# Performance work log

Measured on AMD Instinct MI355X. Metric: run time of the kernel, lower is better.

The kernel has to match this reference:

```python
import jax, jax.numpy as jnp
import numpy as np

NEG_INF = -1.0e9  # matches the torch code's -1000000000.0 fill


def setup_inputs() -> dict:
    key = jax.random.key(0)
    k1, k2, k3, k4 = jax.random.split(key, 4)
    B, Lq, Lk, D = 8, 2048, 2048, 128
    queries = jax.random.normal(k1, (B, Lq, D), dtype=jnp.float32)
    keys = jax.random.normal(k2, (B, Lk, D), dtype=jnp.float32)
    values = jax.random.normal(k3, (B, Lk, D), dtype=jnp.float32)
    valid_length = jax.random.randint(k4, (B,), 1, Lk + 1, dtype=jnp.int32)
    return {"queries": queries, "keys": keys, "values": values,
            "valid_length": valid_length}


def reference(queries, keys, values, valid_length):
    d = queries.shape[-1]
    # scores: [B, Lq, Lk]
    scores = jnp.einsum("bqd,bkd->bqk", queries, keys) / jnp.sqrt(
        jnp.asarray(d, dtype=queries.dtype))
    # per-batch valid key length broadcast over all queries
    Lk = scores.shape[-1]
    mask = jnp.arange(Lk)[None, None, :] >= valid_length[:, None, None]  # [B,1,Lk]
    scores = jnp.where(mask, NEG_INF, scores)
    attn = jax.nn.softmax(scores, axis=-1)
    # dropout p=0.0 -> identity (eval-equivalent)
    return jnp.einsum("bqk,bkd->bqd", attn, values)
```

## Files before the change

### kernel.cpp

```cpp
#include <hip/hip_runtime.h>


#define NB     8
#define LQ     2048
#define LK     2048
#define DH     128
#define KT     32
#define NSPLIT 4
#define CHUNK  512
#define TPS    16
#define NTILES 64
#define SCL2E  0.12751744f

typedef float f32x4 __attribute__((ext_vector_type(4)));
typedef __bf16 bf16x8 __attribute__((ext_vector_type(8)));
typedef unsigned short u16x4 __attribute__((ext_vector_type(4)));
typedef unsigned short u16x8 __attribute__((ext_vector_type(8)));
typedef unsigned int u32x4 __attribute__((ext_vector_type(4)));

#define KWS_OFF   0ull
#define VWS_OFF   (4ull << 20)
#define OPART_OFF (8ull << 20)
#define ML_OFF    (OPART_OFF + (32ull << 20))
#define WS_NEED   (ML_OFF + 262144ull)

static __device__ __forceinline__ unsigned short f2bf(float f) {
    unsigned int u = __builtin_bit_cast(unsigned int, f);
    u += 0x7FFFu + ((u >> 16) & 1u);
    return (unsigned short)(u >> 16);
}

static __device__ __forceinline__ unsigned int cvtpk(float lo, float hi) {
    unsigned int r;
    asm("v_cvt_pk_bf16_f32 %0, %1, %2" : "=v"(r) : "v"(lo), "v"(hi));
    return r;
}

__global__ __launch_bounds__(256)
void prepass(const float* __restrict__ Kg, const float* __restrict__ Vg,
             const int* __restrict__ VLg,
             unsigned short* __restrict__ Kws, unsigned short* __restrict__ Vws) {
    __shared__ unsigned short Kl[KT][136];
    __shared__ unsigned short Vt[DH][40];
    const int tid = threadIdx.x;
    const int b = blockIdx.x >> 6;
    const int t = blockIdx.x & 63;
    if (t * KT >= VLg[b]) return;
    const size_t gbase = ((size_t)b * LK + (size_t)t * KT) * DH;
    const size_t tbase = (size_t)(b * NTILES + t) * 4096;
    #pragma unroll
    for (int i = 0; i < 4; ++i) {
        int e4 = tid + 256 * i;
        int row = e4 >> 5;
        int c4 = (e4 & 31) * 4;
        float4 kv = *reinterpret_cast<const float4*>(Kg + gbase + (size_t)row * DH + c4);
        u16x4 uk = { f2bf(kv.x), f2bf(kv.y), f2bf(kv.z), f2bf(kv.w) };
        *reinterpret_cast<u16x4*>(&Kl[row][c4]) = uk;
        float4 vv = *reinterpret_cast<const float4*>(Vg + gbase + (size_t)row * DH + c4);
        Vt[c4 + 0][row] = f2bf(vv.x);
        Vt[c4 + 1][row] = f2bf(vv.y);
        Vt[c4 + 2][row] = f2bf(vv.z);
        Vt[c4 + 3][row] = f2bf(vv.w);
    }
    __syncthreads();
    #pragma unroll
    for (int i = 0; i < 2; ++i) {
        int u = tid + 256 * i;
        int sl = u >> 6;
        int l = u & 63;
        int krow = 2 * (l & 15) + (sl & 1);
        int kcol = (sl >> 1) * 32 + (l >> 4) * 8;
        u16x8 kk = *reinterpret_cast<const u16x8*>(&Kl[krow][kcol]);
        *reinterpret_cast<u16x8*>(Kws + tbase + u * 8) = kk;
        int vcol = sl * 16 + (l & 15);
        int k0 = (l >> 4) * 8;
        u16x8 vv8 = *reinterpret_cast<const u16x8*>(&Vt[vcol][k0]);
        *reinterpret_cast<u16x8*>(Vws + tbase + u * 8) = vv8;
    }
}

__global__ __launch_bounds__(128, 2)
void attn_split(const float* __restrict__ Qg, const int* __restrict__ VLg,
                const unsigned short* __restrict__ Kws,
                const unsigned short* __restrict__ Vws,
                float* __restrict__ Opart, float* __restrict__ Ml,
                float* __restrict__ Og) {
    __shared__ __align__(16) char shbuf[16640];

    const int tid  = threadIdx.x;
    const int lane = tid & 63;
    const int wv   = tid >> 6;
    const int r    = lane & 15;
    const int grp  = lane >> 4;

    unsigned short* Plds = reinterpret_cast<unsigned short*>(shbuf) + wv * 1280;

    const int bid = blockIdx.x;
    const int b  = bid >> 8;
    const int s  = (bid >> 6) & 3;
    const int qb = bid & 63;

    const int vl = VLg[b];
    if (s * CHUNK >= vl) return;
    int vrem = vl - s * CHUNK;
    if (vrem > CHUNK) vrem = CHUNK;
    const int nt = (vrem + 31) >> 5;
    const bool anymask = (vrem & 31) != 0;
    const int q0 = qb * 32;

    bf16x8 qf0[4], qf1[4];
    #pragma unroll
    for (int rb = 0; rb < 2; ++rb) {
        const float* qrow = Qg + ((size_t)(b * LQ + q0 + rb * 16 + r)) * DH + grp * 8;
        #pragma unroll
        for (int c = 0; c < 4; ++c) {
            float4 f0 = *reinterpret_cast<const float4*>(qrow + c * 32);
            float4 f1 = *reinterpret_cast<const float4*>(qrow + c * 32 + 4);
            u32x4 tw;
            tw[0] = cvtpk(f0.x * SCL2E, f0.y * SCL2E);
            tw[1] = cvtpk(f0.z * SCL2E, f0.w * SCL2E);
            tw[2] = cvtpk(f1.x * SCL2E, f1.y * SCL2E);
            tw[3] = cvtpk(f1.z * SCL2E, f1.w * SCL2E);
            if (rb == 0) qf0[c] = __builtin_bit_cast(bf16x8, tw);
            else         qf1[c] = __builtin_bit_cast(bf16x8, tw);
        }
    }

    const f32x4 zero4 = {0.f, 0.f, 0.f, 0.f};
    f32x4 acc[2][8];
    #pragma unroll
    for (int rb = 0; rb < 2; ++rb)
        #pragma unroll
        for (int d8 = 0; d8 < 8; ++d8) acc[rb][d8] = zero4;
    float lsum[2][4] = {{0.f, 0.f, 0.f, 0.f}, {0.f, 0.f, 0.f, 0.f}};

    const unsigned short* kp =
        Kws + (size_t)(b * NTILES + s * TPS + wv) * 4096 + lane * 8;
    const unsigned short* vp =
        Vws + (size_t)(b * NTILES + s * TPS + wv) * 4096 + lane * 8;

    bf16x8 kreg[8], vreg[8];
    #pragma unroll
    for (int sl = 0; sl < 8; ++sl) {
        kreg[sl] = *reinterpret_cast<const bf16x8*>(kp + sl * 512);
        vreg[sl] = *reinterpret_cast<const bf16x8*>(vp + sl * 512);
    }

    for (int t = wv; t < nt; t += 2) {
        const bool lastt = (t == nt - 1);
        f32x4 s00 = zero4, s01 = zero4, s10 = zero4, s11 = zero4;
        #pragma unroll
        for (int c = 0; c < 4; ++c) {
            s00 = __builtin_amdgcn_mfma_f32_16x16x32_bf16(qf0[c], kreg[2 * c],     s00, 0, 0, 0);
            s01 = __builtin_amdgcn_mfma_f32_16x16x32_bf16(qf0[c], kreg[2 * c + 1], s01, 0, 0, 0);
            s10 = __builtin_amdgcn_mfma_f32_16x16x32_bf16(qf1[c], kreg[2 * c],     s10, 0, 0, 0);
            s11 = __builtin_amdgcn_mfma_f32_16x16x32_bf16(qf1[c], kreg[2 * c + 1], s11, 0, 0, 0);
        }
        if (t + 2 < nt) {
            kp += 2 * 4096;
            #pragma unroll
            for (int sl = 0; sl < 8; ++sl)
                kreg[sl] = *reinterpret_cast<const bf16x8*>(kp + sl * 512);
        }

        const int kk = s * CHUNK + t * KT + 2 * r;
        const bool mm = lastt & anymask;
        const bool m0 = mm && (kk >= vl);
        const bool m1 = mm && (kk + 1 >= vl);
        #pragma unroll
        for (int j = 0; j < 4; ++j) {
            float a0 = m0 ? -1e9f : s00[j];
            float a1 = m1 ? -1e9f : s01[j];
            float b0 = m0 ? -1e9f : s10[j];
            float b1 = m1 ? -1e9f : s11[j];
            float p00 = exp2f(a0), p01 = exp2f(a1);
            float p10 = exp2f(b0), p11 = exp2f(b1);
            lsum[0][j] += p00 + p01;
            lsum[1][j] += p10 + p11;
            *reinterpret_cast<unsigned int*>(&Plds[(grp * 4 + j) * 40 + 2 * r]) =
                cvtpk(p00, p01);
            *reinterpret_cast<unsigned int*>(&Plds[640 + (grp * 4 + j) * 40 + 2 * r]) =
                cvtpk(p10, p11);
        }
        bf16x8 pa0 = *reinterpret_cast<const bf16x8*>(&Plds[r * 40 + grp * 8]);
        bf16x8 pa1 = *reinterpret_cast<const bf16x8*>(&Plds[640 + r * 40 + grp * 8]);

        #pragma unroll
        for (int d8 = 0; d8 < 8; ++d8) {
            acc[0][d8] = __builtin_amdgcn_mfma_f32_16x16x32_bf16(pa0, vreg[d8], acc[0][d8], 0, 0, 0);
            acc[1][d8] = __builtin_amdgcn_mfma_f32_16x16x32_bf16(pa1, vreg[d8], acc[1][d8], 0, 0, 0);
        }
        if (t + 2 < nt) {
            vp += 2 * 4096;
            #pragma unroll
            for (int sl = 0; sl < 8; ++sl)
                vreg[sl] = *reinterpret_cast<const bf16x8*>(vp + sl * 512);
        }
    }

    #pragma unroll
    for (int rb = 0; rb < 2; ++rb) {
        #pragma unroll
        for (int j = 0; j < 4; ++j) {
            float v = lsum[rb][j];
            #pragma unroll
            for (int d = 1; d < 16; d <<= 1) v += __shfl_xor(v, d);
            lsum[rb][j] = v;
        }
    }

    __syncthreads();
    float* Cmb = reinterpret_cast<float*>(shbuf);
    float* Ls  = reinterpret_cast<float*>(shbuf + 16384);
    if (wv == 1) {
        #pragma unroll
        for (int rb = 0; rb < 2; ++rb) {
            #pragma unroll
            for (int d8 = 0; d8 < 8; ++d8) {
                int ps = ((rb * 8 + d8) + lane) & 15;
                *reinterpret_cast<f32x4*>(&Cmb[lane * 64 + ps * 4]) = acc[rb][d8];
            }
        }
        if (r == 0) {
            #pragma unroll
            for (int rb = 0; rb < 2; ++rb)
                #pragma unroll
                for (int j = 0; j < 4; ++j)
                    Ls[rb * 16 + grp * 4 + j] = lsum[rb][j];
        }
    }
    __syncthreads();
    if (wv != 0) return;

    #pragma unroll
    for (int rb = 0; rb < 2; ++rb) {
        #pragma unroll
        for (int d8 = 0; d8 < 8; ++d8) {
            int ps = ((rb * 8 + d8) + lane) & 15;
            f32x4 o = *reinterpret_cast<const f32x4*>(&Cmb[lane * 64 + ps * 4]);
            acc[rb][d8] += o;
        }
        #pragma unroll
        for (int j = 0; j < 4; ++j) lsum[rb][j] += Ls[rb * 16 + grp * 4 + j];
    }

    if (vl <= CHUNK) {
        #pragma unroll
        for (int rb = 0; rb < 2; ++rb)
            #pragma unroll
            for (int d8 = 0; d8 < 8; ++d8)
                #pragma unroll
                for (int j = 0; j < 4; ++j)
                    Og[((size_t)(b * LQ + q0 + rb * 16 + grp * 4 + j)) * 128 + d8 * 16 + r] =
                        acc[rb][d8][j] / lsum[rb][j];
    } else {
        const size_t pbase = (size_t)(b * NSPLIT + s) * LQ;
        #pragma unroll
        for (int rb = 0; rb < 2; ++rb)
            #pragma unroll
            for (int d8 = 0; d8 < 8; ++d8)
                #pragma unroll
                for (int j = 0; j < 4; ++j)
                    Opart[(pbase + q0 + rb * 16 + grp * 4 + j) * 128 + d8 * 16 + r] =
                        acc[rb][d8][j];
        if (r == 0) {
            #pragma unroll
            for (int rb = 0; rb < 2; ++rb)
                #pragma unroll
                for (int j = 0; j < 4; ++j)
                    Ml[pbase + q0 + rb * 16 + grp * 4 + j] = lsum[rb][j];
        }
    }
}

__global__ __launch_bounds__(256)
void reduce_split(const float* __restrict__ Opart, const float* __restrict__ Ml,
                  const int* __restrict__ VLg, float* __restrict__ Og) {
    const int row = blockIdx.x * 8 + (threadIdx.x >> 5);
    const int b = row >> 11;
    const int q = row & 2047;
    const int d4 = (threadIdx.x & 31) * 4;
    const int vl = VLg[b];
    const int ns = min(NSPLIT, (vl + CHUNK - 1) >> 9);
    if (ns <= 1) return;
    float L = 0.f;
    float4 o = {0.f, 0.f, 0.f, 0.f};
    for (int s = 0; s < ns; ++s) {
        size_t i = (size_t)(b * NSPLIT + s) * LQ + q;
        L += Ml[i];
        float4 p = *reinterpret_cast<const float4*>(Opart + i * 128 + d4);
        o.x += p.x; o.y += p.y; o.z += p.z; o.w += p.w;
    }
    float inv = 1.0f / L;
    float4 res = {o.x * inv, o.y * inv, o.z * inv, o.w * inv};
    *reinterpret_cast<float4*>(Og + ((size_t)b * LQ + q) * 128 + d4) = res;
}

#define SCALE 0.08838834764831845f
__global__ __launch_bounds__(256)
void attn_fwd(const float* __restrict__ Qg, const float* __restrict__ Kg,
              const float* __restrict__ Vg, const int* __restrict__ VLg,
              float* __restrict__ Og) {
    __shared__ unsigned short Klds[KT][DH];
    __shared__ unsigned short Vt[DH][KT];
    __shared__ unsigned short Pl[4][16][KT];
    const int tid = threadIdx.x;
    const int lane = tid & 63;
    const int wv = tid >> 6;
    const int r = lane & 15;
    const int grp = lane >> 4;
    const int qblocks = LQ / 64;
    const int b = blockIdx.x / qblocks;
    const int qb = blockIdx.x % qblocks;
    const int q0 = qb * 64 + wv * 16;
    const int vl = VLg[b];
    const int ntiles = (vl + KT - 1) / KT;
    bf16x8 qf[4];
    {
        const float* qrow = Qg + ((size_t)(b * LQ + q0 + r)) * DH + grp * 8;
        #pragma unroll
        for (int c = 0; c < 4; ++c) {
            float4 f0 = *reinterpret_cast<const float4*>(qrow + c * 32);
            float4 f1 = *reinterpret_cast<const float4*>(qrow + c * 32 + 4);
            u16x8 t;
            t[0] = f2bf(f0.x); t[1] = f2bf(f0.y); t[2] = f2bf(f0.z); t[3] = f2bf(f0.w);
            t[4] = f2bf(f1.x); t[5] = f2bf(f1.y); t[6] = f2bf(f1.z); t[7] = f2bf(f1.w);
            qf[c] = __builtin_bit_cast(bf16x8, t);
        }
    }
    const f32x4 zero4 = {0.f, 0.f, 0.f, 0.f};
    f32x4 acc[8];
    #pragma unroll
    for (int d8 = 0; d8 < 8; ++d8) acc[d8] = zero4;
    float mrun[4] = {-1e30f, -1e30f, -1e30f, -1e30f};
    float lsum[4] = {0.f, 0.f, 0.f, 0.f};
    for (int t = 0; t < ntiles; ++t) {
        const int kb = t * KT;
        __syncthreads();
        {
            const size_t kvbase = ((size_t)b * LK + kb) * DH;
            #pragma unroll
            for (int i = 0; i < 4; ++i) {
                int e4 = tid + 256 * i;
                int row = e4 >> 5;
                int c4 = (e4 & 31) * 4;
                float4 kv = *reinterpret_cast<const float4*>(Kg + kvbase + (size_t)row * DH + c4);
                u16x4 uk = { f2bf(kv.x), f2bf(kv.y), f2bf(kv.z), f2bf(kv.w) };
                *reinterpret_cast<u16x4*>(&Klds[row][c4]) = uk;
                float4 vv = *reinterpret_cast<const float4*>(Vg + kvbase + (size_t)row * DH + c4);
                Vt[c4 + 0][row] = f2bf(vv.x);
                Vt[c4 + 1][row] = f2bf(vv.y);
                Vt[c4 + 2][row] = f2bf(vv.z);
                Vt[c4 + 3][row] = f2bf(vv.w);
            }
        }
        __syncthreads();
        f32x4 s0 = zero4, s1 = zero4;
        #pragma unroll
        for (int c = 0; c < 4; ++c) {
            bf16x8 k0 = *reinterpret_cast<const bf16x8*>(&Klds[r][c * 32 + grp * 8]);
            bf16x8 k1 = *reinterpret_cast<const bf16x8*>(&Klds[16 + r][c * 32 + grp * 8]);
            s0 = __builtin_amdgcn_mfma_f32_16x16x32_bf16(qf[c], k0, s0, 0, 0, 0);
            s1 = __builtin_amdgcn_mfma_f32_16x16x32_bf16(qf[c], k1, s1, 0, 0, 0);
        }
        const bool msk0 = (kb + r) >= vl;
        const bool msk1 = (kb + 16 + r) >= vl;
        float alpha[4];
        #pragma unroll
        for (int j = 0; j < 4; ++j) {
            float v0 = msk0 ? -1e9f : s0[j] * SCALE;
            float v1 = msk1 ? -1e9f : s1[j] * SCALE;
            float mx = fmaxf(v0, v1);
            #pragma unroll
            for (int d = 1; d < 16; d <<= 1) mx = fmaxf(mx, __shfl_xor(mx, d));
            float mnew = fmaxf(mrun[j], mx);
            float a = __expf(mrun[j] - mnew);
            float p0 = __expf(v0 - mnew);
            float p1 = __expf(v1 - mnew);
            float rs = p0 + p1;
            #pragma unroll
            for (int d = 1; d < 16; d <<= 1) rs += __shfl_xor(rs, d);
            lsum[j] = lsum[j] * a + rs;
            mrun[j] = mnew;
            alpha[j] = a;
            Pl[wv][grp * 4 + j][r] = f2bf(p0);
            Pl[wv][grp * 4 + j][16 + r] = f2bf(p1);
        }
        #pragma unroll
        for (int d8 = 0; d8 < 8; ++d8) {
            #pragma unroll
            for (int j = 0; j < 4; ++j) acc[d8][j] *= alpha[j];
        }
        bf16x8 pa = *reinterpret_cast<const bf16x8*>(&Pl[wv][r][grp * 8]);
        #pragma unroll
        for (int d8 = 0; d8 < 8; ++d8) {
            bf16x8 vf = *reinterpret_cast<const bf16x8*>(&Vt[d8 * 16 + r][grp * 8]);
            acc[d8] = __builtin_amdgcn_mfma_f32_16x16x32_bf16(pa, vf, acc[d8], 0, 0, 0);
        }
    }
    #pragma unroll
    for (int d8 = 0; d8 < 8; ++d8) {
        #pragma unroll
        for (int j = 0; j < 4; ++j) {
            int qr = q0 + grp * 4 + j;
            Og[((size_t)b * LQ + qr) * DH + d8 * 16 + r] = acc[d8][j] / lsum[j];
        }
    }
}

extern "C" void kernel_launch(void* const* d_in, const int* in_sizes, int n_in,
                              void* d_out, int out_size, void* d_ws, size_t ws_size,
                              hipStream_t stream) {
    const float* Q  = (const float*)d_in[0];
    const float* K  = (const float*)d_in[1];
    const float* V  = (const float*)d_in[2];
    const int*   VL = (const int*)d_in[3];
    float* O = (float*)d_out;

    if (ws_size < WS_NEED) {
        dim3 grid(NB * (LQ / 64));
        attn_fwd<<<grid, 256, 0, stream>>>(Q, K, V, VL, O);
        return;
    }
    unsigned short* Kws = (unsigned short*)((char*)d_ws + KWS_OFF);
    unsigned short* Vws = (unsigned short*)((char*)d_ws + VWS_OFF);
    float* Opart = (float*)((char*)d_ws + OPART_OFF);
    float* Ml    = (float*)((char*)d_ws + ML_OFF);

    prepass<<<dim3(NB * NTILES), 256, 0, stream>>>(K, V, VL, Kws, Vws);
    attn_split<<<dim3(NB * NSPLIT * 64), 128, 0, stream>>>(
        Q, VL, Kws, Vws, Opart, Ml, O);
    reduce_split<<<dim3(NB * LQ / 8), 256, 0, stream>>>(Opart, Ml, VL, O);
}
```

Baseline: 43.05 us.

## Replace split-K attention with single 4-wave block per query tile, reduce in LDS

```diff
diff --git a/kernel.cpp b/kernel.cpp
--- a/kernel.cpp
+++ b/kernel.cpp
@@ -6,9 +6,6 @@
 #define LK     2048
 #define DH     128
 #define KT     32
-#define NSPLIT 4
-#define CHUNK  512
-#define TPS    16
 #define NTILES 64
 #define SCL2E  0.12751744f
 
@@ -20,9 +17,7 @@
 
 #define KWS_OFF   0ull
 #define VWS_OFF   (4ull << 20)
-#define OPART_OFF (8ull << 20)
-#define ML_OFF    (OPART_OFF + (32ull << 20))
-#define WS_NEED   (ML_OFF + 262144ull)
+#define WS_NEED   (8ull << 20)
 
 static __device__ __forceinline__ unsigned short f2bf(float f) {
     unsigned int u = __builtin_bit_cast(unsigned int, f);
@@ -79,13 +74,12 @@
     }
 }
 
-__global__ __launch_bounds__(128, 2)
-void attn_split(const float* __restrict__ Qg, const int* __restrict__ VLg,
-                const unsigned short* __restrict__ Kws,
-                const unsigned short* __restrict__ Vws,
-                float* __restrict__ Opart, float* __restrict__ Ml,
-                float* __restrict__ Og) {
-    __shared__ __align__(16) char shbuf[16640];
+__global__ __launch_bounds__(256, 2)
+void attn_full(const float* __restrict__ Qg, const int* __restrict__ VLg,
+               const unsigned short* __restrict__ Kws,
+               const unsigned short* __restrict__ Vws,
+               float* __restrict__ Og) {
+    __shared__ __align__(16) char shbuf[33024];
 
     const int tid  = threadIdx.x;
     const int lane = tid & 63;
@@ -96,16 +90,12 @@
     unsigned short* Plds = reinterpret_cast<unsigned short*>(shbuf) + wv * 1280;
 
     const int bid = blockIdx.x;
-    const int b  = bid >> 8;
-    const int s  = (bid >> 6) & 3;
+    const int b  = bid >> 6;
     const int qb = bid & 63;
 
     const int vl = VLg[b];
-    if (s * CHUNK >= vl) return;
-    int vrem = vl - s * CHUNK;
-    if (vrem > CHUNK) vrem = CHUNK;
-    const int nt = (vrem + 31) >> 5;
-    const bool anymask = (vrem & 31) != 0;
+    const int nt = (vl + 31) >> 5;
+    const bool anymask = (vl & 31) != 0;
     const int q0 = qb * 32;
 
     bf16x8 qf0[4], qf1[4];
@@ -134,19 +124,19 @@
         for (int d8 = 0; d8 < 8; ++d8) acc[rb][d8] = zero4;
     float lsum[2][4] = {{0.f, 0.f, 0.f, 0.f}, {0.f, 0.f, 0.f, 0.f}};
 
-    const unsigned short* kp =
-        Kws + (size_t)(b * NTILES + s * TPS + wv) * 4096 + lane * 8;
-    const unsigned short* vp =
-        Vws + (size_t)(b * NTILES + s * TPS + wv) * 4096 + lane * 8;
+    const unsigned short* kp = Kws + (size_t)(b * NTILES + wv) * 4096 + lane * 8;
+    const unsigned short* vp = Vws + (size_t)(b * NTILES + wv) * 4096 + lane * 8;
 
     bf16x8 kreg[8], vreg[8];
-    #pragma unroll
-    for (int sl = 0; sl < 8; ++sl) {
-        kreg[sl] = *reinterpret_cast<const bf16x8*>(kp + sl * 512);
-        vreg[sl] = *reinterpret_cast<const bf16x8*>(vp + sl * 512);
-    }
-
-    for (int t = wv; t < nt; t += 2) {
+    if (wv < nt) {
+        #pragma unroll
+        for (int sl = 0; sl < 8; ++sl) {
+            kreg[sl] = *reinterpret_cast<const bf16x8*>(kp + sl * 512);
+            vreg[sl] = *reinterpret_cast<const bf16x8*>(vp + sl * 512);
+        }
+    }
+
+    for (int t = wv; t < nt; t += 4) {
         const bool lastt = (t == nt - 1);
         f32x4 s00 = zero4, s01 = zero4, s10 = zero4, s11 = zero4;
         #pragma unroll
@@ -156,14 +146,14 @@
             s10 = __builtin_amdgcn_mfma_f32_16x16x32_bf16(qf1[c], kreg[2 * c],     s10, 0, 0, 0);
             s11 = __builtin_amdgcn_mfma_f32_16x16x32_bf16(qf1[c], kreg[2 * c + 1], s11, 0, 0, 0);
         }
-        if (t + 2 < nt) {
-            kp += 2 * 4096;
+        if (t + 4 < nt) {
+            kp += 4 * 4096;
             #pragma unroll
             for (int sl = 0; sl < 8; ++sl)
                 kreg[sl] = *reinterpret_cast<const bf16x8*>(kp + sl * 512);
         }
 
-        const int kk = s * CHUNK + t * KT + 2 * r;
+        const int kk = t * KT + 2 * r;
         const bool mm = lastt & anymask;
         const bool m0 = mm && (kk >= vl);
         const bool m1 = mm && (kk + 1 >= vl);
@@ -190,8 +180,8 @@
             acc[0][d8] = __builtin_amdgcn_mfma_f32_16x16x32_bf16(pa0, vreg[d8], acc[0][d8], 0, 0, 0);
             acc[1][d8] = __builtin_amdgcn_mfma_f32_16x16x32_bf16(pa1, vreg[d8], acc[1][d8], 0, 0, 0);
         }
-        if (t + 2 < nt) {
-            vp += 2 * 4096;
+        if (t + 4 < nt) {
+            vp += 4 * 4096;
             #pragma unroll
             for (int sl = 0; sl < 8; ++sl)
                 vreg[sl] = *reinterpret_cast<const bf16x8*>(vp + sl * 512);
@@ -209,25 +199,47 @@
         }
     }
 
+    float* A  = reinterpret_cast<float*>(shbuf);
+    float* Bz = reinterpret_cast<float*>(shbuf + 16384);
+    float* Ls = reinterpret_cast<float*>(shbuf + 32768);
     __syncthreads();
-    float* Cmb = reinterpret_cast<float*>(shbuf);
-    float* Ls  = reinterpret_cast<float*>(shbuf + 16384);
-    if (wv == 1) {
-        #pragma unroll
-        for (int rb = 0; rb < 2; ++rb) {
+    if (wv == 1 || wv == 3) {
+        float* R = (wv == 1) ? A : Bz;
+        #pragma unroll
+        for (int rb = 0; rb < 2; ++rb)
             #pragma unroll
             for (int d8 = 0; d8 < 8; ++d8) {
                 int ps = ((rb * 8 + d8) + lane) & 15;
-                *reinterpret_cast<f32x4*>(&Cmb[lane * 64 + ps * 4]) = acc[rb][d8];
+                *reinterpret_cast<f32x4*>(&R[lane * 64 + ps * 4]) = acc[rb][d8];
             }
-        }
-        if (r == 0) {
-            #pragma unroll
-            for (int rb = 0; rb < 2; ++rb)
-                #pragma unroll
-                for (int j = 0; j < 4; ++j)
-                    Ls[rb * 16 + grp * 4 + j] = lsum[rb][j];
-        }
+    }
+    if (wv != 0 && r == 0) {
+        #pragma unroll
+        for (int rb = 0; rb < 2; ++rb)
+            #pragma unroll
+            for (int j = 0; j < 4; ++j)
+                Ls[(wv - 1) * 32 + rb * 16 + grp * 4 + j] = lsum[rb][j];
+    }
+    __syncthreads();
+    if (wv == 0 || wv == 2) {
+        const float* R = (wv == 0) ? A : Bz;
+        #pragma unroll
+        for (int rb = 0; rb < 2; ++rb)
+            #pragma unroll
+            for (int d8 = 0; d8 < 8; ++d8) {
+                int ps = ((rb * 8 + d8) + lane) & 15;
+                acc[rb][d8] += *reinterpret_cast<const f32x4*>(&R[lane * 64 + ps * 4]);
+            }
+    }
+    __syncthreads();
+    if (wv == 2) {
+        #pragma unroll
+        for (int rb = 0; rb < 2; ++rb)
+            #pragma unroll
+            for (int d8 = 0; d8 < 8; ++d8) {
+                int ps = ((rb * 8 + d8) + lane) & 15;
+                *reinterpret_cast<f32x4*>(&A[lane * 64 + ps * 4]) = acc[rb][d8];
+            }
     }
     __syncthreads();
     if (wv != 0) return;
@@ -237,63 +249,22 @@
         #pragma unroll
         for (int d8 = 0; d8 < 8; ++d8) {
             int ps = ((rb * 8 + d8) + lane) & 15;
-            f32x4 o = *reinterpret_cast<const f32x4*>(&Cmb[lane * 64 + ps * 4]);
-            acc[rb][d8] += o;
-        }
-        #pragma unroll
-        for (int j = 0; j < 4; ++j) lsum[rb][j] += Ls[rb * 16 + grp * 4 + j];
-    }
-
-    if (vl <= CHUNK) {
-        #pragma unroll
-        for (int rb = 0; rb < 2; ++rb)
-            #pragma unroll
-            for (int d8 = 0; d8 < 8; ++d8)
-                #pragma unroll
-                for (int j = 0; j < 4; ++j)
-                    Og[((size_t)(b * LQ + q0 + rb * 16 + grp * 4 + j)) * 128 + d8 * 16 + r] =
-                        acc[rb][d8][j] / lsum[rb][j];
-    } else {
-        const size_t pbase = (size_t)(b * NSPLIT + s) * LQ;
-        #pragma unroll
-        for (int rb = 0; rb < 2; ++rb)
-            #pragma unroll
-            for (int d8 = 0; d8 < 8; ++d8)
-                #pragma unroll
-                for (int j = 0; j < 4; ++j)
-                    Opart[(pbase + q0 + rb * 16 + grp * 4 + j) * 128 + d8 * 16 + r] =
-                        acc[rb][d8][j];
-        if (r == 0) {
-            #pragma unroll
-            for (int rb = 0; rb < 2; ++rb)
-                #pragma unroll
-                for (int j = 0; j < 4; ++j)
-                    Ml[pbase + q0 + rb * 16 + grp * 4 + j] = lsum[rb][j];
-        }
-    }
-}
-
-__global__ __launch_bounds__(256)
-void reduce_split(const float* __restrict__ Opart, const float* __restrict__ Ml,
-                  const int* __restrict__ VLg, float* __restrict__ Og) {
-    const int row = blockIdx.x * 8 + (threadIdx.x >> 5);
-    const int b = row >> 11;
-    const int q = row & 2047;
-    const int d4 = (threadIdx.x & 31) * 4;
-    const int vl = VLg[b];
-    const int ns = min(NSPLIT, (vl + CHUNK - 1) >> 9);
-    if (ns <= 1) return;
-    float L = 0.f;
-    float4 o = {0.f, 0.f, 0.f, 0.f};
-    for (int s = 0; s < ns; ++s) {
-        size_t i = (size_t)(b * NSPLIT + s) * LQ + q;
-        L += Ml[i];
-        float4 p = *reinterpret_cast<const float4*>(Opart + i * 128 + d4);
-        o.x += p.x; o.y += p.y; o.z += p.z; o.w += p.w;
-    }
-    float inv = 1.0f / L;
-    float4 res = {o.x * inv, o.y * inv, o.z * inv, o.w * inv};
-    *reinterpret_cast<float4*>(Og + ((size_t)b * LQ + q) * 128 + d4) = res;
+            acc[rb][d8] += *reinterpret_cast<const f32x4*>(&A[lane * 64 + ps * 4]);
+        }
+        #pragma unroll
+        for (int j = 0; j < 4; ++j)
+            lsum[rb][j] += Ls[rb * 16 + grp * 4 + j] + Ls[32 + rb * 16 + grp * 4 + j]
+                         + Ls[64 + rb * 16 + grp * 4 + j];
+    }
+
+    #pragma unroll
+    for (int rb = 0; rb < 2; ++rb)
+        #pragma unroll
+        for (int d8 = 0; d8 < 8; ++d8)
+            #pragma unroll
+            for (int j = 0; j < 4; ++j)
+                Og[((size_t)(b * LQ + q0 + rb * 16 + grp * 4 + j)) * 128 + d8 * 16 + r] =
+                    acc[rb][d8][j] / lsum[rb][j];
 }
 
 #define SCALE 0.08838834764831845f
@@ -424,11 +395,7 @@
     }
     unsigned short* Kws = (unsigned short*)((char*)d_ws + KWS_OFF);
     unsigned short* Vws = (unsigned short*)((char*)d_ws + VWS_OFF);
-    float* Opart = (float*)((char*)d_ws + OPART_OFF);
-    float* Ml    = (float*)((char*)d_ws + ML_OFF);
 
     prepass<<<dim3(NB * NTILES), 256, 0, stream>>>(K, V, VL, Kws, Vws);
-    attn_split<<<dim3(NB * NSPLIT * 64), 128, 0, stream>>>(
-        Q, VL, Kws, Vws, Opart, Ml, O);
-    reduce_split<<<dim3(NB * LQ / 8), 256, 0, stream>>>(Opart, Ml, VL, O);
-}
+    attn_full<<<dim3(NB * 64), 256, 0, stream>>>(Q, VL, Kws, Vws, O);
+}
```

New measurement: 39.30 us. 1.1x faster.
